# Kernel tuning notes

Measured on AMD Instinct MI355X. Metric: run time of the kernel, lower is better.

The kernel has to match this reference:

```python
import jax, jax.numpy as jnp
import numpy as np

H = 768
NH = 12
HD = H // NH  # 64


def setup_inputs() -> dict:
    key = jax.random.key(0)
    ks = jax.random.split(key, 10)
    B, S = 8, 1024
    x = jax.random.normal(ks[0], (B, S, H), dtype=jnp.float32)
    attention_mask = jax.random.randint(ks[1], (B, S), 0, 2, dtype=jnp.int32)
    s = 1.0 / np.sqrt(H)
    Wq = jax.random.normal(ks[2], (H, H), jnp.float32) * s
    bq = jnp.zeros((H,), jnp.float32)
    Wk = jax.random.normal(ks[3], (H, H), jnp.float32) * s
    bk = jnp.zeros((H,), jnp.float32)
    Wv = jax.random.normal(ks[4], (H, H), jnp.float32) * s
    bv = jnp.zeros((H,), jnp.float32)
    Wo = jax.random.normal(ks[5], (H, H), jnp.float32) * s
    bo = jnp.zeros((H,), jnp.float32)
    return {"x": x, "attention_mask": attention_mask,
            "Wq": Wq, "bq": bq, "Wk": Wk, "bk": bk,
            "Wv": Wv, "bv": bv, "Wo": Wo, "bo": bo}


def reference(x, attention_mask, Wq, bq, Wk, bk, Wv, bv, Wo, bo):
    B, S, _ = x.shape
    scale = HD ** -0.5
    # projections -> [B, NH, S, HD]
    def split_heads(t):
        return t.reshape(B, S, NH, HD).transpose(0, 2, 1, 3)
    q = split_heads(x @ Wq.T + bq)
    k = split_heads(x @ Wk.T + bk)
    v = split_heads(x @ Wv.T + bv)
    scores = jnp.einsum('bhqd,bhkd->bhqk', q, k) * scale  # [B,NH,S,S]
    mask = attention_mask[:, None, None, :]  # [B,1,1,S]
    scores = jnp.where(mask == 0, jnp.float32(-10000.0), scores)
    probs = jax.nn.softmax(scores, axis=-1)
    ctx = jnp.einsum('bhqk,bhkd->bhqd', probs, v)  # [B,NH,S,HD]
    ctx = ctx.transpose(0, 2, 1, 3).reshape(B, S, H)
    out = ctx @ Wo.T + bo
    return out
```

## Files before the change

kernel.cpp:

```cpp
#include <hip/hip_runtime.h>
#include <hip/hip_bf16.h>

#define HDIM 768
#define NH 12
#define HD 64
#define BB 8
#define SS 1024
#define MROWS (BB*SS)
#define NQKV (3*HDIM)
#define GK 768

#define SCL2E 0.18033688011f
#define MASKNEG -14426.9504f

typedef __attribute__((ext_vector_type(8))) short bf16x8;
typedef __attribute__((ext_vector_type(4))) float f32x4;

__device__ __forceinline__ unsigned short f2bf(float f) {
    unsigned int u = __float_as_uint(f);
    unsigned int r = (u + 0x7fffu + ((u >> 16) & 1u)) >> 16;
    return (unsigned short)r;
}

__device__ __forceinline__ void gload_lds16(const void* gsrc, void* ldst) {
    __builtin_amdgcn_global_load_lds(
        (const __attribute__((address_space(1))) unsigned int*)gsrc,
        (__attribute__((address_space(3))) unsigned int*)ldst,
        16, 0, 0);
}

__global__ void pack_all(const float* __restrict__ x,
                         const float* __restrict__ Wq, const float* __restrict__ Wk,
                         const float* __restrict__ Wv, const float* __restrict__ Wo,
                         const float* __restrict__ bq, const float* __restrict__ bk,
                         const float* __restrict__ bv, const int* __restrict__ m,
                         unsigned short* __restrict__ xb, unsigned short* __restrict__ wqkv,
                         unsigned short* __restrict__ wo,
                         float* __restrict__ biasq, float* __restrict__ madd)
{
    const int tid = blockIdx.x * blockDim.x + threadIdx.x;
    const int stride = gridDim.x * blockDim.x;
    for (int i = tid; i < 2162688; i += stride) {
        const float* src; unsigned short* dst; int off;
        if (i < 1572864) { src = x; dst = xb; off = i; }
        else {
            int j = i - 1572864;
            int seg = j / 147456;
            off = j - seg * 147456;
            src = (seg == 0) ? Wq : (seg == 1) ? Wk : (seg == 2) ? Wv : Wo;
            dst = (seg == 3) ? wo : wqkv + seg * (HDIM * HDIM);
        }
        float4 v = reinterpret_cast<const float4*>(src)[off];
        union { unsigned short u[4]; unsigned long long q; } o;
        o.u[0] = f2bf(v.x); o.u[1] = f2bf(v.y); o.u[2] = f2bf(v.z); o.u[3] = f2bf(v.w);
        reinterpret_cast<unsigned long long*>(dst)[off] = o.q;
    }
    if (tid < 3 * HDIM)
        biasq[tid] = (tid < HDIM) ? bq[tid] : (tid < 2 * HDIM) ? bk[tid - HDIM] : bv[tid - 2 * HDIM];
    if (tid < BB * SS)
        madd[tid] = (m[tid] == 0) ? MASKNEG : 0.0f;
}

template<int MODE>
__global__ __launch_bounds__(512)
void gemm_bt(const unsigned short* __restrict__ A,
             const unsigned short* __restrict__ Bw,
             const float* __restrict__ bias,
             unsigned short* __restrict__ qb,
             unsigned short* __restrict__ kb,
             unsigned short* __restrict__ vtb,
             float* __restrict__ fout,
             int K, int gridN)
{
    __shared__ unsigned short As[2][128 * 64];
    __shared__ unsigned short Bs[2][128 * 64];
    const int tid  = threadIdx.x;
    const int wave = tid >> 6;
    const int lane = tid & 63;

    const int nwg = gridDim.x;
    const int cpx = nwg >> 3;
    const int wg  = (blockIdx.x & 7) * cpx + (blockIdx.x >> 3);
    const int bm = (wg / gridN) * 128;
    const int bn = (wg % gridN) * 128;

    const int wm = (wave >> 2) * 64;
    const int wn = (wave & 3) * 32;
    const int lr  = lane & 15;
    const int hv  = lane >> 4;
    const int e3  = lr & 7;
    const int srow = lane >> 3;
    const int sg   = lane & 7;

    f32x4 zero4 = {0.f, 0.f, 0.f, 0.f};
    f32x4 acc[4][2];
#pragma unroll
    for (int i = 0; i < 4; i++)
#pragma unroll
        for (int j = 0; j < 2; j++) acc[i][j] = zero4;

    auto stage = [&](int buf, int k0) {
        const int gk = (sg ^ srow) * 8;
#pragma unroll
        for (int jj = 0; jj < 2; ++jj) {
            int i = wave * 2 + jj;
            gload_lds16(A  + (size_t)(bm + i * 8 + srow) * K + k0 + gk, &As[buf][i * 8 * 64]);
            gload_lds16(Bw + (size_t)(bn + i * 8 + srow) * K + k0 + gk, &Bs[buf][i * 8 * 64]);
        }
    };

    stage(0, 0);
    if (K > 64) stage(1, 64);

    int buf = 0;
    for (int k0 = 0; k0 < K; k0 += 64) {
        if (k0 + 64 < K) { asm volatile("s_waitcnt vmcnt(4)" ::: "memory"); }
        else             { asm volatile("s_waitcnt vmcnt(0)" ::: "memory"); }
        __builtin_amdgcn_s_barrier();
        __builtin_amdgcn_sched_barrier(0);

        bf16x8 af[4][2], bf[2][2];
#pragma unroll
        for (int mi = 0; mi < 4; mi++)
#pragma unroll
            for (int kk = 0; kk < 2; kk++)
                af[mi][kk] = *(const bf16x8*)
                    &As[buf][(wm + mi * 16 + lr) * 64 + ((kk * 4 + hv) ^ e3) * 8];
#pragma unroll
        for (int ni = 0; ni < 2; ni++)
#pragma unroll
            for (int kk = 0; kk < 2; kk++)
                bf[ni][kk] = *(const bf16x8*)
                    &Bs[buf][(wn + ni * 16 + lr) * 64 + ((kk * 4 + hv) ^ e3) * 8];

        __builtin_amdgcn_s_setprio(1);
#pragma unroll
        for (int kk = 0; kk < 2; kk++)
#pragma unroll
            for (int mi = 0; mi < 4; mi++)
#pragma unroll
                for (int ni = 0; ni < 2; ni++)
                    acc[mi][ni] = __builtin_amdgcn_mfma_f32_16x16x32_bf16(
                        af[mi][kk], bf[ni][kk], acc[mi][ni], 0, 0, 0);
        __builtin_amdgcn_s_setprio(0);

        __builtin_amdgcn_s_barrier();
        if (k0 + 128 < K) stage(buf, k0 + 128);
        buf ^= 1;
    }

    const int rgrp = lane >> 4;
#pragma unroll
    for (int mi = 0; mi < 4; mi++)
#pragma unroll
        for (int ni = 0; ni < 2; ni++)
#pragma unroll
            for (int r = 0; r < 4; r++) {
                int m = bm + wm + mi * 16 + rgrp * 4 + r;
                int n = bn + wn + ni * 16 + lr;
                float v = acc[mi][ni][r] + bias[n];
                if (MODE == 0) {
                    int which = n / HDIM;
                    int nn = n - which * HDIM;
                    int h = nn >> 6, d = nn & 63;
                    int b = m >> 10, s = m & 1023;
                    unsigned short bvv = f2bf(v);
                    if (which == 0)      qb [(((size_t)(b * NH + h)) * SS + s) * HD + d] = bvv;
                    else if (which == 1) kb [(((size_t)(b * NH + h)) * SS + s) * HD + d] = bvv;
                    else                 vtb[(((size_t)(b * NH + h)) * HD + d) * SS + s] = bvv;
                } else {
                    fout[(size_t)m * HDIM + n] = v;
                }
            }
}

__global__ __launch_bounds__(256, 3)
void attn_kernel(const unsigned short* __restrict__ qb,
                 const unsigned short* __restrict__ kb,
                 const unsigned short* __restrict__ vtb,
                 const float* __restrict__ maskadd,
                 unsigned short* __restrict__ ctx)
{
    __shared__ unsigned short Ks[64][64];
    __shared__ unsigned short Vs[64][64];
    __shared__ unsigned short Ps[4][32][64];

    const int tid  = threadIdx.x;
    const int wave = tid >> 6;
    const int lane = tid & 63;
    const int wg = (blockIdx.x & 7) * 96 + (blockIdx.x >> 3);
    const int qt = wg & 7;
    const int h  = (wg >> 3) % NH;
    const int b  = wg / 96;
    const int bh = b * NH + h;
    const int q0 = qt * 128 + wave * 32;
    const int lr  = lane & 15;
    const int hi  = lane >> 4;
    const int e3  = lr & 7;
    const int srow = lane >> 3;
    const int sg   = lane & 7;

    const unsigned short* Qp = qb  + (size_t)bh * SS * HD;
    const unsigned short* Kp = kb  + (size_t)bh * SS * HD;
    const unsigned short* Vp = vtb + (size_t)bh * HD * SS;
    const float* madd = maskadd + b * SS;

    bf16x8 aq[2][2];
#pragma unroll
    for (int g = 0; g < 2; g++)
#pragma unroll
        for (int kk = 0; kk < 2; kk++)
            aq[g][kk] = *(const bf16x8*)&Qp[(size_t)(q0 + g * 16 + lr) * HD + kk * 32 + hi * 8];

    f32x4 zero4 = {0.f, 0.f, 0.f, 0.f};
    f32x4 o[2][4];
#pragma unroll
    for (int g = 0; g < 2; g++)
#pragma unroll
        for (int i = 0; i < 4; i++) o[g][i] = zero4;
    float plsum0 = 0.f, plsum1 = 0.f;

    bf16x8 kreg[2], vreg[2];
    auto ld = [&](int t0) {
#pragma unroll
        for (int jj = 0; jj < 2; ++jj) {
            int rr = (wave * 2 + jj) * 8 + srow;
            kreg[jj] = *(const bf16x8*)&Kp[(size_t)(t0 + rr) * HD + sg * 8];
            vreg[jj] = *(const bf16x8*)&Vp[(size_t)rr * SS + t0 + sg * 8];
        }
    };
    auto wr = [&]() {
        const int slot = (sg ^ srow) * 8;
#pragma unroll
        for (int jj = 0; jj < 2; ++jj) {
            int rr = (wave * 2 + jj) * 8 + srow;
            *(bf16x8*)&Ks[rr][slot] = kreg[jj];
            *(bf16x8*)&Vs[rr][slot] = vreg[jj];
        }
    };

    ld(0);
    wr();
    __syncthreads();

    for (int t0 = 0; t0 < SS; t0 += 64) {
        const bool more = (t0 + 64 < SS);
        if (more) ld(t0 + 64);

        f32x4 sacc[2][4];
#pragma unroll
        for (int g = 0; g < 2; g++)
#pragma unroll
            for (int ni = 0; ni < 4; ni++) sacc[g][ni] = zero4;
        __builtin_amdgcn_s_setprio(1);
#pragma unroll
        for (int kk = 0; kk < 2; kk++)
#pragma unroll
            for (int ni = 0; ni < 4; ni++) {
                bf16x8 kf = *(const bf16x8*)&Ks[ni * 16 + lr][((kk * 4 + hi) ^ e3) * 8];
                sacc[0][ni] = __builtin_amdgcn_mfma_f32_16x16x32_bf16(kf, aq[0][kk], sacc[0][ni], 0, 0, 0);
                sacc[1][ni] = __builtin_amdgcn_mfma_f32_16x16x32_bf16(kf, aq[1][kk], sacc[1][ni], 0, 0, 0);
            }
        __builtin_amdgcn_s_setprio(0);

        float4 md[4];
#pragma unroll
        for (int ni = 0; ni < 4; ni++)
            md[ni] = *(const float4*)&madd[t0 + ni * 16 + hi * 4];

#pragma unroll
        for (int ni = 0; ni < 4; ni++) {
            float p0 = __builtin_amdgcn_exp2f(fmaf(sacc[0][ni][0], SCL2E, md[ni].x));
            float p1 = __builtin_amdgcn_exp2f(fmaf(sacc[0][ni][1], SCL2E, md[ni].y));
            float p2 = __builtin_amdgcn_exp2f(fmaf(sacc[0][ni][2], SCL2E, md[ni].z));
            float p3 = __builtin_amdgcn_exp2f(fmaf(sacc[0][ni][3], SCL2E, md[ni].w));
            plsum0 += p0 + p1 + p2 + p3;
            union { __hip_bfloat162 h2[2]; unsigned long long q; } u;
            u.h2[0] = __float22bfloat162_rn(make_float2(p0, p1));
            u.h2[1] = __float22bfloat162_rn(make_float2(p2, p3));
            *(unsigned long long*)&Ps[wave][lr][((4 * ni + hi) ^ (e3 << 1)) * 4] = u.q;
        }
#pragma unroll
        for (int ni = 0; ni < 4; ni++) {
            float p0 = __builtin_amdgcn_exp2f(fmaf(sacc[1][ni][0], SCL2E, md[ni].x));
            float p1 = __builtin_amdgcn_exp2f(fmaf(sacc[1][ni][1], SCL2E, md[ni].y));
            float p2 = __builtin_amdgcn_exp2f(fmaf(sacc[1][ni][2], SCL2E, md[ni].z));
            float p3 = __builtin_amdgcn_exp2f(fmaf(sacc[1][ni][3], SCL2E, md[ni].w));
            plsum1 += p0 + p1 + p2 + p3;
            union { __hip_bfloat162 h2[2]; unsigned long long q; } u;
            u.h2[0] = __float22bfloat162_rn(make_float2(p0, p1));
            u.h2[1] = __float22bfloat162_rn(make_float2(p2, p3));
            *(unsigned long long*)&Ps[wave][16 + lr][((4 * ni + hi) ^ (e3 << 1)) * 4] = u.q;
        }

        __builtin_amdgcn_s_setprio(1);
#pragma unroll
        for (int ks = 0; ks < 2; ks++) {
            bf16x8 pa0 = *(const bf16x8*)&Ps[wave][lr]     [((8 * ks + 2 * hi) ^ (e3 << 1)) * 4];
            bf16x8 pa1 = *(const bf16x8*)&Ps[wave][16 + lr][((8 * ks + 2 * hi) ^ (e3 << 1)) * 4];
#pragma unroll
            for (int nd = 0; nd < 4; nd++) {
                bf16x8 vb = *(const bf16x8*)&Vs[nd * 16 + lr][((4 * ks + hi) ^ e3) * 8];
                o[0][nd] = __builtin_amdgcn_mfma_f32_16x16x32_bf16(pa0, vb, o[0][nd], 0, 0, 0);
                o[1][nd] = __builtin_amdgcn_mfma_f32_16x16x32_bf16(pa1, vb, o[1][nd], 0, 0, 0);
            }
        }
        __builtin_amdgcn_s_setprio(0);

        __syncthreads();
        if (more) {
            wr();
            __syncthreads();
        }
    }

#pragma unroll
    for (int g = 0; g < 2; g++) {
        float lrun = (g == 0) ? plsum0 : plsum1;
        lrun += __shfl_xor(lrun, 16);
        lrun += __shfl_xor(lrun, 32);
        float iv[4];
#pragma unroll
        for (int r = 0; r < 4; r++) iv[r] = 1.0f / __shfl(lrun, hi * 4 + r, 16);
#pragma unroll
        for (int r = 0; r < 4; r++) {
            int grow = b * SS + q0 + g * 16 + hi * 4 + r;
#pragma unroll
            for (int nd = 0; nd < 4; nd++)
                ctx[(size_t)grow * HDIM + h * HD + nd * 16 + lr] =
                    f2bf(((g == 0) ? o[0][nd][r] : o[1][nd][r]) * iv[r]);
        }
    }
}

extern "C" void kernel_launch(void* const* d_in, const int* in_sizes, int n_in,
                              void* d_out, int out_size, void* d_ws, size_t ws_size,
                              hipStream_t stream)
{
    const float* x    = (const float*)d_in[0];
    const int*   amask= (const int*)d_in[1];
    const float* Wq   = (const float*)d_in[2];
    const float* bq   = (const float*)d_in[3];
    const float* Wk   = (const float*)d_in[4];
    const float* bk   = (const float*)d_in[5];
    const float* Wv   = (const float*)d_in[6];
    const float* bv   = (const float*)d_in[7];
    const float* Wo   = (const float*)d_in[8];
    const float* bo   = (const float*)d_in[9];
    float* out = (float*)d_out;

    char* ws = (char*)d_ws;
    unsigned short* xb   = (unsigned short*)(ws);
    unsigned short* wqkv = (unsigned short*)(ws + 12582912);
    unsigned short* wo   = (unsigned short*)(ws + 16121856);
    float*          biasq= (float*)(ws + 17301504);
    unsigned short* qb   = (unsigned short*)(ws + 17310720);
    unsigned short* kb   = (unsigned short*)(ws + 29893632);
    unsigned short* vtb  = (unsigned short*)(ws + 42476544);
    unsigned short* ctx  = (unsigned short*)(ws + 55059456);
    float*          madd = (float*)(ws + 67642368);

    pack_all<<<2048, 256, 0, stream>>>(x, Wq, Wk, Wv, Wo, bq, bk, bv, amask,
                                       xb, wqkv, wo, biasq, madd);

    gemm_bt<0><<<(MROWS / 128) * (NQKV / 128), 512, 0, stream>>>(
        xb, wqkv, biasq, qb, kb, vtb, nullptr, GK, NQKV / 128);

    attn_kernel<<<(SS / 128) * NH * BB, 256, 0, stream>>>(qb, kb, vtb, madd, ctx);

    gemm_bt<1><<<(MROWS / 128) * (HDIM / 128), 512, 0, stream>>>(
        ctx, wo, bo, nullptr, nullptr, nullptr, out, GK, HDIM / 128);
}
```

Measured before the change: 128.9 us.

## Pre-swizzle x and Wqkv into MFMA fragment layout and use LDS-free QKV GEMM

The pack kernel now writes x and the QKV weights in a tiled layout where each 16-row by 8-element granule is contiguous, matching the MFMA operand fragment order. A new QKV GEMM kernel loads fragments straight from global memory into registers with no LDS staging or barriers, using 256-thread blocks with 64x64 tiles per wave. This removes LDS traffic and synchronisation, but it relies on L2/cache reuse for the repeated operand loads and has no software prefetch across k-steps. The output projection keeps the old LDS-based GEMM, now specialised to plain fp32 output.

```diff
diff --git a/kernel.cpp b/kernel.cpp
--- a/kernel.cpp
+++ b/kernel.cpp
@@ -9,6 +9,7 @@
 #define MROWS (BB*SS)
 #define NQKV (3*HDIM)
 #define GK 768
+#define NGRAN 96
 
 #define SCL2E 0.18033688011f
 #define MASKNEG -14426.9504f
@@ -34,26 +35,46 @@
                          const float* __restrict__ Wv, const float* __restrict__ Wo,
                          const float* __restrict__ bq, const float* __restrict__ bk,
                          const float* __restrict__ bv, const int* __restrict__ m,
-                         unsigned short* __restrict__ xb, unsigned short* __restrict__ wqkv,
+                         unsigned short* __restrict__ xbf, unsigned short* __restrict__ wqkvf,
                          unsigned short* __restrict__ wo,
                          float* __restrict__ biasq, float* __restrict__ madd)
 {
     const int tid = blockIdx.x * blockDim.x + threadIdx.x;
     const int stride = gridDim.x * blockDim.x;
-    for (int i = tid; i < 2162688; i += stride) {
-        const float* src; unsigned short* dst; int off;
-        if (i < 1572864) { src = x; dst = xb; off = i; }
-        else {
-            int j = i - 1572864;
-            int seg = j / 147456;
-            off = j - seg * 147456;
-            src = (seg == 0) ? Wq : (seg == 1) ? Wk : (seg == 2) ? Wv : Wo;
-            dst = (seg == 3) ? wo : wqkv + seg * (HDIM * HDIM);
-        }
-        float4 v = reinterpret_cast<const float4*>(src)[off];
-        union { unsigned short u[4]; unsigned long long q; } o;
-        o.u[0] = f2bf(v.x); o.u[1] = f2bf(v.y); o.u[2] = f2bf(v.z); o.u[3] = f2bf(v.w);
-        reinterpret_cast<unsigned long long*>(dst)[off] = o.q;
+    for (int i = tid; i < 1155072; i += stride) {
+        if (i < 1007616) {
+            int row, g;
+            const float* srcrow;
+            unsigned short* dst;
+            if (i < 786432) {
+                row = i / NGRAN; g = i - row * NGRAN;
+                srcrow = x + (size_t)row * GK;
+                dst = xbf;
+            } else {
+                int j = i - 786432;
+                row = j / NGRAN; g = j - row * NGRAN;
+                int which = row / HDIM, rr = row - which * HDIM;
+                srcrow = ((which == 0) ? Wq : (which == 1) ? Wk : Wv) + (size_t)rr * GK;
+                dst = wqkvf;
+            }
+            float4 v0 = *(const float4*)(srcrow + g * 8);
+            float4 v1 = *(const float4*)(srcrow + g * 8 + 4);
+            unsigned long long q0 =
+                (unsigned long long)f2bf(v0.x) | ((unsigned long long)f2bf(v0.y) << 16)
+              | ((unsigned long long)f2bf(v0.z) << 32) | ((unsigned long long)f2bf(v0.w) << 48);
+            unsigned long long q1 =
+                (unsigned long long)f2bf(v1.x) | ((unsigned long long)f2bf(v1.y) << 16)
+              | ((unsigned long long)f2bf(v1.z) << 32) | ((unsigned long long)f2bf(v1.w) << 48);
+            unsigned long long* p = (unsigned long long*)
+                (dst + ((size_t)(row >> 4) * NGRAN + g) * 128 + (row & 15) * 8);
+            p[0] = q0; p[1] = q1;
+        } else {
+            int off = i - 1007616;
+            float4 v = reinterpret_cast<const float4*>(Wo)[off];
+            union { unsigned short u[4]; unsigned long long q; } o;
+            o.u[0] = f2bf(v.x); o.u[1] = f2bf(v.y); o.u[2] = f2bf(v.z); o.u[3] = f2bf(v.w);
+            reinterpret_cast<unsigned long long*>(wo)[off] = o.q;
+        }
     }
     if (tid < 3 * HDIM)
         biasq[tid] = (tid < HDIM) ? bq[tid] : (tid < 2 * HDIM) ? bk[tid - HDIM] : bv[tid - 2 * HDIM];
@@ -61,14 +82,89 @@
         madd[tid] = (m[tid] == 0) ? MASKNEG : 0.0f;
 }
 
-template<int MODE>
+__global__ __launch_bounds__(256, 3)
+void gemm_flat(const unsigned short* __restrict__ Af,
+               const unsigned short* __restrict__ Bf,
+               const float* __restrict__ bias,
+               unsigned short* __restrict__ qb,
+               unsigned short* __restrict__ kb,
+               unsigned short* __restrict__ vtb)
+{
+    const int tid  = threadIdx.x;
+    const int wave = tid >> 6;
+    const int lane = tid & 63;
+
+    const int nwg = gridDim.x;
+    const int cpx = nwg >> 3;
+    const int wg  = (blockIdx.x & 7) * cpx + (blockIdx.x >> 3);
+    const int bm = (wg / 18) * 128;
+    const int bn = (wg % 18) * 128;
+
+    const int wm = (wave >> 1) * 64;
+    const int wn = (wave & 1) * 64;
+    const int lr = lane & 15;
+    const int hv = lane >> 4;
+
+    const unsigned short* Abase = Af + ((size_t)((bm + wm) >> 4) * NGRAN) * 128 + hv * 128 + lr * 8;
+    const unsigned short* Bbase = Bf + ((size_t)((bn + wn) >> 4) * NGRAN) * 128 + hv * 128 + lr * 8;
+
+    f32x4 zero4 = {0.f, 0.f, 0.f, 0.f};
+    f32x4 acc[4][4];
+#pragma unroll
+    for (int i = 0; i < 4; i++)
+#pragma unroll
+        for (int j = 0; j < 4; j++) acc[i][j] = zero4;
+
+    for (int t = 0; t < 12; ++t) {
+        bf16x8 af[4][2], bf[4][2];
+#pragma unroll
+        for (int mi = 0; mi < 4; mi++)
+#pragma unroll
+            for (int kk = 0; kk < 2; kk++)
+                af[mi][kk] = *(const bf16x8*)(Abase + ((size_t)mi * NGRAN + t * 8 + kk * 4) * 128);
+#pragma unroll
+        for (int ni = 0; ni < 4; ni++)
+#pragma unroll
+            for (int kk = 0; kk < 2; kk++)
+                bf[ni][kk] = *(const bf16x8*)(Bbase + ((size_t)ni * NGRAN + t * 8 + kk * 4) * 128);
+
+        __builtin_amdgcn_s_setprio(1);
+#pragma unroll
+        for (int kk = 0; kk < 2; kk++)
+#pragma unroll
+            for (int mi = 0; mi < 4; mi++)
+#pragma unroll
+                for (int ni = 0; ni < 4; ni++)
+                    acc[mi][ni] = __builtin_amdgcn_mfma_f32_16x16x32_bf16(
+                        af[mi][kk], bf[ni][kk], acc[mi][ni], 0, 0, 0);
+        __builtin_amdgcn_s_setprio(0);
+    }
+
+    const int rgrp = lane >> 4;
+#pragma unroll
+    for (int mi = 0; mi < 4; mi++)
+#pragma unroll
+        for (int ni = 0; ni < 4; ni++)
+#pragma unroll
+            for (int r = 0; r < 4; r++) {
+                int m = bm + wm + mi * 16 + rgrp * 4 + r;
+                int n = bn + wn + ni * 16 + lr;
+                float v = acc[mi][ni][r] + bias[n];
+                int which = n / HDIM;
+                int nn = n - which * HDIM;
+                int h = nn >> 6, d = nn & 63;
+                int b = m >> 10, s = m & 1023;
+                unsigned short bvv = f2bf(v);
+                if (which == 0)      qb [(((size_t)(b * NH + h)) * SS + s) * HD + d] = bvv;
+                else if (which == 1) kb [(((size_t)(b * NH + h)) * SS + s) * HD + d] = bvv;
+                else                 vtb[(((size_t)(b * NH + h)) * HD + d) * SS + s] = bvv;
+            }
+}
+
 __global__ __launch_bounds__(512)
 void gemm_bt(const unsigned short* __restrict__ A,
              const unsigned short* __restrict__ Bw,
              const float* __restrict__ bias,
-             unsigned short* __restrict__ qb,
-             unsigned short* __restrict__ kb,
-             unsigned short* __restrict__ vtb,
              float* __restrict__ fout,
              int K, int gridN)
 {
@@ -158,19 +254,7 @@
             for (int r = 0; r < 4; r++) {
                 int m = bm + wm + mi * 16 + rgrp * 4 + r;
                 int n = bn + wn + ni * 16 + lr;
-                float v = acc[mi][ni][r] + bias[n];
-                if (MODE == 0) {
-                    int which = n / HDIM;
-                    int nn = n - which * HDIM;
-                    int h = nn >> 6, d = nn & 63;
-                    int b = m >> 10, s = m & 1023;
-                    unsigned short bvv = f2bf(v);
-                    if (which == 0)      qb [(((size_t)(b * NH + h)) * SS + s) * HD + d] = bvv;
-                    else if (which == 1) kb [(((size_t)(b * NH + h)) * SS + s) * HD + d] = bvv;
-                    else                 vtb[(((size_t)(b * NH + h)) * HD + d) * SS + s] = bvv;
-                } else {
-                    fout[(size_t)m * HDIM + n] = v;
-                }
+                fout[(size_t)m * HDIM + n] = acc[mi][ni][r] + bias[n];
             }
 }
 
@@ -350,8 +434,8 @@
     float* out = (float*)d_out;
 
     char* ws = (char*)d_ws;
-    unsigned short* xb   = (unsigned short*)(ws);
-    unsigned short* wqkv = (unsigned short*)(ws + 12582912);
+    unsigned short* xbf  = (unsigned short*)(ws);
+    unsigned short* wqkvf= (unsigned short*)(ws + 12582912);
     unsigned short* wo   = (unsigned short*)(ws + 16121856);
     float*          biasq= (float*)(ws + 17301504);
     unsigned short* qb   = (unsigned short*)(ws + 17310720);
@@ -361,13 +445,13 @@
     float*          madd = (float*)(ws + 67642368);
 
     pack_all<<<2048, 256, 0, stream>>>(x, Wq, Wk, Wv, Wo, bq, bk, bv, amask,
-                                       xb, wqkv, wo, biasq, madd);
-
-    gemm_bt<0><<<(MROWS / 128) * (NQKV / 128), 512, 0, stream>>>(
-        xb, wqkv, biasq, qb, kb, vtb, nullptr, GK, NQKV / 128);
+                                       xbf, wqkvf, wo, biasq, madd);
+
+    gemm_flat<<<(MROWS / 128) * (NQKV / 128), 256, 0, stream>>>(
+        xbf, wqkvf, biasq, qb, kb, vtb);
 
     attn_kernel<<<(SS / 128) * NH * BB, 256, 0, stream>>>(qb, kb, vtb, madd, ctx);
 
-    gemm_bt<1><<<(MROWS / 128) * (HDIM / 128), 512, 0, stream>>>(
-        ctx, wo, bo, nullptr, nullptr, nullptr, out, GK, HDIM / 128);
-}
+    gemm_bt<<<(MROWS / 128) * (HDIM / 128), 512, 0, stream>>>(
+        ctx, wo, bo, out, GK, HDIM / 128);
+}
```

New measurement: 138.5 us. 7.4% more time.
